# Kernel optimization log

Measured on AMD Instinct MI355X. Metric: run time of the kernel, lower is better.

Reference implementation:

```python
import jax, jax.numpy as jnp
import numpy as np

MAXT = 10000
BATCH = 4096
LOG_GAMMA = float(np.log(1.02))
ALPHA = float(np.log(0.99) / 1000.0)
INIT_LOGW = float(np.log(0.248))
INIT_LOGP = float(np.log(0.001))
TEMPERATURE = 1000.0
EPS = 1e-12


def setup_inputs() -> dict:
    key = jax.random.key(0)
    k1, k2 = jax.random.split(key)
    # actions are initialized to -10 in the original module (must be << 0 so exp(a) < 1)
    acts = -10.0 * jnp.ones((MAXT,), dtype=jnp.float32)
    u1 = jax.random.uniform(k1, (MAXT, BATCH), dtype=jnp.float32)
    u2 = jax.random.uniform(k2, (MAXT, BATCH), dtype=jnp.float32)
    return {"acts": acts, "u1": u1, "u2": u2}


def _gumbel_sigmoid(logp, uu1, uu2):
    # logit = logp - log(1 - exp(logp))
    logit = logp - jnp.log1p(-jnp.exp(logp))
    noise = -jnp.log(jnp.log(uu2 + EPS) / jnp.log(uu1 + EPS) + EPS)
    soft = jax.nn.sigmoid(logit + noise)  # gumbel_temp = 1
    hard = (soft > 0.5).astype(soft.dtype)
    # straight-through: hard value, soft gradient
    return soft + jax.lax.stop_gradient(hard - soft)


def reference(acts, u1, u2):
    def step(carry, xs):
        logp, logw, alive, cumrew = carry
        a, uu1, uu2 = xs
        alive = alive * (1.0 - _gumbel_sigmoid(logp, uu1, uu2))
        f = jnp.exp(a)
        new_logw = logw + LOG_GAMMA + jnp.log(1.0 - f)
        new_logp = logp + ALPHA * f * jnp.exp(logw)
        rwd = alive * jnp.exp(new_logw / TEMPERATURE)
        return (new_logp, new_logw, alive, cumrew + rwd), None

    batch = u1.shape[1]
    init = (
        jnp.full((batch,), INIT_LOGP, dtype=jnp.float32),
        jnp.full((batch,), INIT_LOGW, dtype=jnp.float32),
        jnp.ones((batch,), dtype=jnp.float32),
        jnp.zeros((batch,), dtype=jnp.float32),
    )
    (_, _, _, cumrew), _ = jax.lax.scan(step, init, (acts, u1, u2))
    return cumrew.mean()
```

## Files before the change

kernel.cpp:

```cpp
#include <hip/hip_runtime.h>
#include <limits.h>

#define MAXT 10000
#define BATCH 4096
#define NYB 80
#define TCHUNK 16
#define SEGT 1536
#define EPT 6
#define NT2 1024
#define SEG2 10
#define CUT_ODDS 9.3e-13f

#define LOG_GAMMA_C  1.9802627296e-2f
#define ALPHA_C     -1.0050335854e-5f
#define INIT_LOGW_C -1.3943265329f
#define INIT_LOGP_C -6.9077552790f
#define EPS_C        1e-12f

__device__ __forceinline__ float block_exscan_tot(float v, float* sh, int tid,
                                                  int n, float* tot) {
    sh[tid] = v;
    __syncthreads();
    for (int off = 1; off < n; off <<= 1) {
        float x = (tid >= off) ? sh[tid - off] : 0.0f;
        __syncthreads();
        sh[tid] += x;
        __syncthreads();
    }
    float excl = (tid > 0) ? sh[tid - 1] : 0.0f;
    float t_ = sh[n - 1];
    __syncthreads();
    *tot = t_;
    return excl;
}

__device__ __forceinline__ float block_exscan_tot_fast(float v, float* shw,
                                                       int tid, int nwaves,
                                                       float* tot) {
    float s = v;
    #pragma unroll
    for (int o = 1; o < 64; o <<= 1) {
        float x = __shfl_up(s, o, 64);
        if ((tid & 63) >= o) s += x;
    }
    float sprev = __shfl_up(s, 1, 64);
    const int wid = tid >> 6, lane = tid & 63;
    if (lane == 63) shw[wid] = s;
    __syncthreads();
    float wpre = 0.0f, wtot = 0.0f;
    for (int w = 0; w < nwaves; ++w) {
        float x = shw[w];
        wtot += x;
        if (w < wid) wpre += x;
    }
    __syncthreads();
    *tot = wtot;
    return (lane == 0) ? wpre : (wpre + sprev);
}

__global__ __launch_bounds__(256) void scan_fused(
    const float* __restrict__ acts,
    const float* __restrict__ u1, const float* __restrict__ u2,
    unsigned* __restrict__ ff)
{
    __shared__ float sh[256];
    __shared__ int   swmin[4];
    __shared__ float s_gate[SEGT];

    const int tid = threadIdx.x;
    const int b4  = (blockIdx.x * 256 + tid) * 4;
    const float E = EPS_C;

    float carry_w = INIT_LOGW_C;
    float carry_p = INIT_LOGP_C;
    unsigned f0 = MAXT, f1 = MAXT, f2 = MAXT, f3 = MAXT;

    for (int seg_base = 0; seg_base < MAXT; seg_base += SEGT) {
        float fv[EPT], dv[EPT];
        float lsum = 0.0f;
        #pragma unroll
        for (int i = 0; i < EPT; ++i) {
            int t = seg_base + tid * EPT + i;
            if (t < MAXT) {
                float f = expf(acts[t]);
                fv[i] = f;
                dv[i] = LOG_GAMMA_C + logf(1.0f - f);
            } else { fv[i] = 0.0f; dv[i] = 0.0f; }
            lsum += dv[i];
        }
        float dtot;
        float excl = block_exscan_tot(lsum, sh, tid, 256, &dtot);

        float run = carry_w + excl;
        float cv[EPT];
        float csum = 0.0f;
        #pragma unroll
        for (int i = 0; i < EPT; ++i) {
            cv[i] = ALPHA_C * fv[i] * expf(run);
            run += dv[i];
            csum += cv[i];
        }
        float ctot;
        float cexcl = block_exscan_tot(csum, sh, tid, 256, &ctot);

        float logp = carry_p + cexcl;
        int localFirst = INT_MAX;
        #pragma unroll
        for (int i = 0; i < EPT; ++i) {
            int t = seg_base + tid * EPT + i;
            float el   = expf(logp);
            float odds = el / (1.0f - el);
            s_gate[tid * EPT + i] = odds - E;
            if (localFirst == INT_MAX && odds <= CUT_ODDS) localFirst = t;
            logp += cv[i];
        }
        #pragma unroll
        for (int o = 32; o > 0; o >>= 1)
            localFirst = min(localFirst, __shfl_xor(localFirst, o, 64));
        if ((tid & 63) == 0) swmin[tid >> 6] = localFirst;
        __syncthreads();
        const int segcut = min(min(swmin[0], swmin[1]),
                               min(swmin[2], swmin[3]));

        const int tlimit = min(segcut, MAXT);
        for (int lc = 0; lc < SEGT / TCHUNK; ++lc) {
            const int cg = seg_base / TCHUNK + lc;
            if ((cg % NYB) != (int)blockIdx.y) continue;
            const int tstart = seg_base + lc * TCHUNK;
            if (tstart >= tlimit) break;
            #pragma unroll
            for (int g = 0; g < TCHUNK / 4; ++g) {
                float4 a[4], c[4];
                float gv[4];
                #pragma unroll
                for (int j = 0; j < 4; ++j) {
                    const int t = tstart + g * 4 + j;
                    a[j]  = *(const float4*)(u1 + (size_t)t * BATCH + b4);
                    c[j]  = *(const float4*)(u2 + (size_t)t * BATCH + b4);
                    gv[j] = s_gate[t - seg_base];
                }
                #pragma unroll
                for (int j = 0; j < 4; ++j) {
                    const unsigned t = (unsigned)(tstart + g * 4 + j);
                    const float k = gv[j];
                    if (__logf(c[j].x + E) > k * __logf(a[j].x + E)) f0 = min(f0, t);
                    if (__logf(c[j].y + E) > k * __logf(a[j].y + E)) f1 = min(f1, t);
                    if (__logf(c[j].z + E) > k * __logf(a[j].z + E)) f2 = min(f2, t);
                    if (__logf(c[j].w + E) > k * __logf(a[j].w + E)) f3 = min(f3, t);
                }
            }
        }

        if (segcut != INT_MAX) break;
        carry_w += dtot;
        carry_p += ctot;
        __syncthreads();
    }

    if (f0 < MAXT) atomicMin(&ff[b4 + 0], f0);
    if (f1 < MAXT) atomicMin(&ff[b4 + 1], f1);
    if (f2 < MAXT) atomicMin(&ff[b4 + 2], f2);
    if (f3 < MAXT) atomicMin(&ff[b4 + 3], f3);
}

__global__ __launch_bounds__(NT2) void finalize_kernel(
    const float* __restrict__ acts,
    const unsigned* __restrict__ ff,
    float* __restrict__ out)
{
    __shared__ float  shw[16];
    __shared__ double sdw[16];
    __shared__ float  rp[MAXT + 1];
    const int tid = threadIdx.x;

    const unsigned fv0 = ff[tid];
    const unsigned fv1 = ff[tid + NT2];
    const unsigned fv2 = ff[tid + 2 * NT2];
    const unsigned fv3 = ff[tid + 3 * NT2];

    const int t0 = tid * SEG2;
    const int n  = (t0 < MAXT) ? min(SEG2, MAXT - t0) : 0;

    float dv[SEG2];
    float lsum = 0.0f;
    for (int i = 0; i < n; ++i) {
        float f = expf(acts[t0 + i]);
        dv[i] = LOG_GAMMA_C + logf(1.0f - f);
        lsum += dv[i];
    }
    float dtot;
    float excl = block_exscan_tot_fast(lsum, shw, tid, NT2 / 64, &dtot);
    float run = INIT_LOGW_C + excl;

    float rv[SEG2];
    float rsum = 0.0f;
    for (int i = 0; i < n; ++i) {
        run += dv[i];
        rv[i] = expf(run * 1e-3f);
        rsum += rv[i];
    }
    float rtot;
    float rexcl = block_exscan_tot_fast(rsum, shw, tid, NT2 / 64, &rtot);
    float rrun = rexcl;
    for (int i = 0; i < n; ++i) { rp[t0 + i] = rrun; rrun += rv[i]; }
    if (tid == 0) rp[MAXT] = rtot;
    __syncthreads();

    double s = 0.0;
    s += (double)rp[min(fv0, (unsigned)MAXT)];
    s += (double)rp[min(fv1, (unsigned)MAXT)];
    s += (double)rp[min(fv2, (unsigned)MAXT)];
    s += (double)rp[min(fv3, (unsigned)MAXT)];

    #pragma unroll
    for (int o = 32; o > 0; o >>= 1) s += __shfl_xor(s, o, 64);
    if ((tid & 63) == 0) sdw[tid >> 6] = s;
    __syncthreads();
    if (tid == 0) {
        double t_ = 0.0;
        for (int w = 0; w < NT2 / 64; ++w) t_ += sdw[w];
        out[0] = (float)(t_ / (double)BATCH);
    }
}

extern "C" void kernel_launch(void* const* d_in, const int* in_sizes, int n_in,
                              void* d_out, int out_size, void* d_ws, size_t ws_size,
                              hipStream_t stream) {
    const float* acts = (const float*)d_in[0];
    const float* u1   = (const float*)d_in[1];
    const float* u2   = (const float*)d_in[2];
    float* out = (float*)d_out;

    unsigned* ff = (unsigned*)d_ws;

    hipMemsetAsync(ff, 0xFF, BATCH * sizeof(unsigned), stream);

    dim3 grid(BATCH / (256 * 4), NYB);
    scan_fused<<<grid, 256, 0, stream>>>(acts, u1, u2, ff);
    finalize_kernel<<<1, NT2, 0, stream>>>(acts, ff, out);
}
```

Before: 280.5 us.

## Skip u1 loads via per-step u2 threshold prefilter and double-buffer block scan

For each timestep the kernel now precomputes a threshold on u2 such that, when all u2 values fall below it, no death event is possible, because log(u1) is bounded below for float inputs. Only when some u2 in a float4 exceeds the threshold is u1 loaded and the exact log comparison run, which aims to roughly halve global memory traffic in this bandwidth-bound kernel. All 16 u2 loads per chunk are issued up front. The block scan is also switched to double-buffered shared memory so each step needs one barrier instead of two. The threshold depends on a hand-chosen bound (27.632 ≈ -log(1e-12)) and a small margin, so correctness rests on that bound staying conservative.

New measurement: 285.5 us. Within noise of the previous version (+1.8%).

```diff
diff --git a/kernel.cpp b/kernel.cpp
--- a/kernel.cpp
+++ b/kernel.cpp
@@ -19,16 +19,19 @@
 
 __device__ __forceinline__ float block_exscan_tot(float v, float* sh, int tid,
                                                   int n, float* tot) {
-    sh[tid] = v;
-    __syncthreads();
+    float s = v;
+    sh[tid] = s;
+    __syncthreads();
+    int src = 0;
     for (int off = 1; off < n; off <<= 1) {
-        float x = (tid >= off) ? sh[tid - off] : 0.0f;
+        float x = (tid >= off) ? sh[src + tid - off] : 0.0f;
+        s += x;
+        sh[(src ^ n) + tid] = s;
         __syncthreads();
-        sh[tid] += x;
-        __syncthreads();
-    }
-    float excl = (tid > 0) ? sh[tid - 1] : 0.0f;
-    float t_ = sh[n - 1];
+        src ^= n;
+    }
+    float excl = (tid > 0) ? sh[src + tid - 1] : 0.0f;
+    float t_ = sh[src + n - 1];
     __syncthreads();
     *tot = t_;
     return excl;
@@ -63,9 +66,10 @@
     const float* __restrict__ u1, const float* __restrict__ u2,
     unsigned* __restrict__ ff)
 {
-    __shared__ float sh[256];
+    __shared__ float sh[512];
     __shared__ int   swmin[4];
     __shared__ float s_gate[SEGT];
+    __shared__ float s_thr[SEGT];
 
     const int tid = threadIdx.x;
     const int b4  = (blockIdx.x * 256 + tid) * 4;
@@ -110,7 +114,10 @@
             int t = seg_base + tid * EPT + i;
             float el   = expf(logp);
             float odds = el / (1.0f - el);
-            s_gate[tid * EPT + i] = odds - E;
+            float k    = odds - E;
+            s_gate[tid * EPT + i] = k;
+            s_thr [tid * EPT + i] =
+                expf(-27.632f * fmaxf(k, 0.0f)) - 1e-6f;
             if (localFirst == INT_MAX && odds <= CUT_ODDS) localFirst = t;
             logp += cv[i];
         }
@@ -128,25 +135,26 @@
             if ((cg % NYB) != (int)blockIdx.y) continue;
             const int tstart = seg_base + lc * TCHUNK;
             if (tstart >= tlimit) break;
+            float4 c[TCHUNK];
+            float gv[TCHUNK], tv[TCHUNK];
             #pragma unroll
-            for (int g = 0; g < TCHUNK / 4; ++g) {
-                float4 a[4], c[4];
-                float gv[4];
-                #pragma unroll
-                for (int j = 0; j < 4; ++j) {
-                    const int t = tstart + g * 4 + j;
-                    a[j]  = *(const float4*)(u1 + (size_t)t * BATCH + b4);
-                    c[j]  = *(const float4*)(u2 + (size_t)t * BATCH + b4);
-                    gv[j] = s_gate[t - seg_base];
-                }
-                #pragma unroll
-                for (int j = 0; j < 4; ++j) {
-                    const unsigned t = (unsigned)(tstart + g * 4 + j);
-                    const float k = gv[j];
-                    if (__logf(c[j].x + E) > k * __logf(a[j].x + E)) f0 = min(f0, t);
-                    if (__logf(c[j].y + E) > k * __logf(a[j].y + E)) f1 = min(f1, t);
-                    if (__logf(c[j].z + E) > k * __logf(a[j].z + E)) f2 = min(f2, t);
-                    if (__logf(c[j].w + E) > k * __logf(a[j].w + E)) f3 = min(f3, t);
+            for (int q = 0; q < TCHUNK; ++q) {
+                const int t = tstart + q;
+                c[q]  = *(const float4*)(u2 + (size_t)t * BATCH + b4);
+                gv[q] = s_gate[t - seg_base];
+                tv[q] = s_thr[t - seg_base];
+            }
+            #pragma unroll
+            for (int q = 0; q < TCHUNK; ++q) {
+                if (c[q].x > tv[q] || c[q].y > tv[q] ||
+                    c[q].z > tv[q] || c[q].w > tv[q]) {
+                    const unsigned t = (unsigned)(tstart + q);
+                    const float k = gv[q];
+                    const float4 a = *(const float4*)(u1 + (size_t)t * BATCH + b4);
+                    if (__logf(c[q].x + E) > k * __logf(a.x + E)) f0 = min(f0, t);
+                    if (__logf(c[q].y + E) > k * __logf(a.y + E)) f1 = min(f1, t);
+                    if (__logf(c[q].z + E) > k * __logf(a.z + E)) f2 = min(f2, t);
+                    if (__logf(c[q].w + E) > k * __logf(a.w + E)) f3 = min(f3, t);
                 }
             }
         }
```
